# Performance work log

Measured on AMD Instinct MI355X. Metric: run time of the kernel, lower is better.

Reference implementation:

```python
import jax, jax.numpy as jnp
import numpy as np
from jax import lax

B, E, DIN = 16, 1024, 128   # batch, num_edges, link_state_dim
P, D = 2048, 128            # num_paths, path_state_dim


def _topology():
    # deterministic ragged paths: lengths in [4,16], at least one of max length 16
    lengths = 4 + (np.arange(P) % 13)
    idx = np.repeat(np.arange(P), lengths).astype(np.int32)          # path id per entry
    seqs = np.concatenate([np.arange(l) for l in lengths]).astype(np.int32)  # position in path
    paths = np.random.RandomState(0).randint(0, E, size=idx.shape[0]).astype(np.int32)
    return paths, idx, seqs


def setup_inputs() -> dict:
    key = jax.random.key(0)
    ks = jax.random.split(key, 8)
    paths, idx, seqs = _topology()
    s_in = 1.0 / np.sqrt(DIN)
    s_h = 1.0 / np.sqrt(D)
    return dict(
        inputs=jax.random.normal(ks[0], (B, E, DIN), jnp.float32),
        W_in=jax.random.normal(ks[1], (DIN, 3 * D), jnp.float32) * s_in,
        W_rec=jax.random.normal(ks[2], (D, 3 * D), jnp.float32) * s_h,
        b_in=jnp.zeros((3 * D,), jnp.float32),
        b_rec=jnp.zeros((3 * D,), jnp.float32),
        wq=jax.random.normal(ks[3], (D, D), jnp.float32) * s_h,
        wk=jax.random.normal(ks[4], (D, D), jnp.float32) * s_h,
        wv=jax.random.normal(ks[5], (D, D), jnp.float32) * s_h,
        paths=paths, idx=idx, seqs=seqs,
    )


def _forward(inputs, W_in, W_rec, b_in, b_rec, wq, wk, wv, paths, idx, seqs, max_len):
    Bc = inputs.shape[0]
    # --- ragged gather -> dense zero-padded tensor [B, P, max_len, DIN] (tf.gather + scatter_nd) ---
    h_tild = inputs[:, paths]                                  # [B, n_entries, DIN]
    link = jnp.zeros((Bc, P, max_len, DIN), inputs.dtype)
    link = link.at[:, idx, seqs].set(h_tild)
    x = link.reshape(Bc * P, max_len, DIN)                     # [BP, L, DIN]
    # --- GRU over time (keras GRUCell default: reset_after=True, tanh/sigmoid) ---
    xg = jnp.einsum('nld,de->lne', x, W_in) + b_in             # [L, BP, 3D]
    h0 = jnp.zeros((Bc * P, D), inputs.dtype)

    def step(h, xg_t):
        hg = h @ W_rec + b_rec                                 # [BP, 3D]
        xz, xr, xh = jnp.split(xg_t, 3, axis=-1)
        hz, hr, hh = jnp.split(hg, 3, axis=-1)
        z = jax.nn.sigmoid(xz + hz)
        r = jax.nn.sigmoid(xr + hr)
        hc = jnp.tanh(xh + r * hh)
        hn = z * h + (1.0 - z) * hc
        return hn, hn

    last, hs = lax.scan(step, h0, xg)                          # last:[BP,D], hs:[L,BP,D]
    hs = jnp.transpose(hs, (1, 0, 2))                          # [BP, L, D]
    # --- single-query QKV attention (raw scores, no softmax, as in source) ---
    key_ = hs @ wk                                             # [BP, L, D]
    val = hs @ wv                                              # [BP, L, D]
    q = last @ wq                                              # [BP, D]
    att = jnp.einsum('nld,nd->nl', key_, q)                    # [BP, L]
    ctx = jnp.einsum('nl,nld->nd', att, val)                   # [BP, D]
    return ctx.reshape(Bc, P, D)


def reference(inputs, W_in, W_rec, b_in, b_rec, wq, wk, wv, paths, idx, seqs):
    max_len = int(np.max(np.asarray(seqs))) + 1                # static (16)
    return _forward(inputs, W_in, W_rec, b_in, b_rec, wq, wk, wv, paths, idx, seqs, max_len)
```

## Files before the change

### kernel.cpp

```cpp
#include <hip/hip_runtime.h>
#include <hip/hip_bf16.h>
#include <cstddef>

#define P_ 2048
#define B_ 16
#define E_ 1024
#define D_ 128
#define L_ 16
#define TD_ 384

typedef _Float16 f16x2 __attribute__((ext_vector_type(2)));
typedef _Float16 f16x8 __attribute__((ext_vector_type(8)));
typedef float    f32x4 __attribute__((ext_vector_type(4)));

__device__ __forceinline__ unsigned short f2h(float x) {
    _Float16 h = (_Float16)x;
    return __builtin_bit_cast(unsigned short, h);
}
__device__ __forceinline__ unsigned pk2(float a, float b) {
    return __builtin_bit_cast(unsigned, __builtin_amdgcn_cvt_pkrtz(a, b));
}

__device__ __forceinline__ void wf16(const float* __restrict__ src,
                                     unsigned short* __restrict__ dst, int g, int N) {
    int lane = g & 63, kt = (g >> 6) & 3, tile = g >> 8;
    int k0 = kt * 32 + (lane >> 4) * 8;
    int c = tile * 16 + (lane & 15);
#pragma unroll
    for (int j = 0; j < 8; ++j)
        dst[(size_t)g * 8 + j] = f2h(src[(size_t)(k0 + j) * N + c]);
}

__global__ __launch_bounds__(256) void k_prep(const float* __restrict__ W_rec,
                                              const float* __restrict__ W_in,
                                              const float* __restrict__ wq,
                                              const float* __restrict__ wk,
                                              const float* __restrict__ wv,
                                              int* __restrict__ pt,
                                              unsigned short* __restrict__ WfR,
                                              unsigned short* __restrict__ WfI,
                                              unsigned short* __restrict__ wvf,
                                              float* __restrict__ M) {
    __shared__ float wk_lds[128 * 129];
    __shared__ float wq_row2[2][128];
    int blk = blockIdx.x, tid = threadIdx.x;
    if      (blk < 128) { pt[blk * 256 + tid] = -1; return; }
    else if (blk < 152) { wf16(W_rec, WfR, (blk - 128) * 256 + tid, TD_); return; }
    else if (blk < 176) { wf16(W_in,  WfI, (blk - 152) * 256 + tid, TD_); return; }
    else if (blk < 184) { wf16(wv,    wvf, (blk - 176) * 256 + tid, 128); return; }
    int j0 = (blk - 184) * 2;
    int d = tid & 127, half = tid >> 7;
    for (int r = half * 64; r < half * 64 + 64; ++r)
        wk_lds[r * 129 + d] = wk[r * 128 + d];
    wq_row2[half][d] = wq[(j0 + half) * 128 + d];
    __syncthreads();
    float acc = 0.f;
    for (int k = 0; k < 128; ++k) acc += wq_row2[half][k] * wk_lds[d * 129 + k];
    M[(j0 + half) * 128 + d] = acc;
}

__global__ __launch_bounds__(256) void k_G(const float* __restrict__ inputs,
                                           const unsigned short* __restrict__ WfI,
                                           const float* __restrict__ b_in,
                                           unsigned short* __restrict__ G2,
                                           const int* __restrict__ paths,
                                           const int* __restrict__ idx,
                                           const int* __restrict__ seqs, int J, int scatB,
                                           int* __restrict__ pt,
                                           const float* __restrict__ M,
                                           unsigned short* __restrict__ Mf) {
    if (blockIdx.x >= 1024) {
        int tb = blockIdx.x - 1024;
        if (tb < scatB) {
            int j = tb * 256 + threadIdx.x;
            if (j < J) pt[idx[j] * L_ + seqs[j]] = paths[j];
        } else {
            wf16(M, Mf, (tb - scatB) * 256 + threadIdx.x, 128);
        }
        return;
    }
    __shared__ __align__(16) unsigned short a_lds[16][136];
    int tid = threadIdx.x, w = tid >> 6, L = tid & 63;
    int l15 = L & 15, q = L >> 4;
    int row0 = blockIdx.x * 16;
    {
        int r = tid >> 4, c = (tid & 15) * 8;
        const float4* p = (const float4*)(inputs + (size_t)(row0 + r) * 128 + c);
        float4 v0 = p[0], v1 = p[1];
        uint4 st;
        st.x = pk2(v0.x, v0.y); st.y = pk2(v0.z, v0.w);
        st.z = pk2(v1.x, v1.y); st.w = pk2(v1.z, v1.w);
        *(uint4*)&a_lds[r][c] = st;
    }
    __syncthreads();
    f16x8 af[4];
#pragma unroll
    for (int kt = 0; kt < 4; ++kt)
        af[kt] = *(const f16x8*)&a_lds[l15][kt * 32 + q * 8];
#pragma unroll
    for (int ct = 0; ct < 6; ++ct) {
        int tl = 6 * w + ct;
        f32x4 acc = (f32x4){0.f, 0.f, 0.f, 0.f};
#pragma unroll
        for (int kt = 0; kt < 4; ++kt)
            acc = __builtin_amdgcn_mfma_f32_16x16x32_f16(
                af[kt], *(const f16x8*)(WfI + (size_t)((tl * 4 + kt) * 64 + L) * 8), acc, 0, 0, 0);
        int g  = tl >> 3;
        int dd = (tl & 7) * 16 + l15;
        float bia = b_in[tl * 16 + l15];
#pragma unroll
        for (int j = 0; j < 4; ++j) {
            int r = q * 4 + j;
            G2[((size_t)(row0 + r) * 128 + dd) * 4 + g] = f2h(acc[j] + bia);
        }
    }
}

__global__ __launch_bounds__(512, 4) void k_rec(const unsigned short* __restrict__ WfR,
                                                const float* __restrict__ b_rec,
                                                const float* __restrict__ b_in,
                                                const unsigned short* __restrict__ G2,
                                                const int* __restrict__ pt,
                                                const unsigned short* __restrict__ Mf,
                                                const unsigned short* __restrict__ wvf,
                                                float* __restrict__ out) {
    __shared__ __align__(16) unsigned short hsl[16][16][136];
    __shared__ __align__(16) unsigned short qkb[16][136];
    __shared__ __align__(16) unsigned short svb[16][136];
    __shared__ float attl[16][20];
    __shared__ int pt_lds[16][16];

    int tid = threadIdx.x, w = tid >> 6, L = tid & 63;
    int l15 = L & 15, q = L >> 4;
    int c = 16 * w + l15;
    int n0 = blockIdx.x * 16;
    int b  = n0 >> 11;
    int p0 = n0 & (P_ - 1);

    f16x8 bfrag[3][4];
#pragma unroll
    for (int g = 0; g < 3; ++g)
#pragma unroll
        for (int kt = 0; kt < 4; ++kt)
            bfrag[g][kt] = *(const f16x8*)(WfR + (size_t)(((g * 8 + w) * 4 + kt) * 64 + L) * 8);

    if (tid < 256) pt_lds[tid >> 4][tid & 15] = pt[p0 * L_ + tid];

    float bz = b_in[c], br = b_in[128 + c], bh = b_in[256 + c];
    float rz = b_rec[c], rr = b_rec[128 + c], rh = b_rec[256 + c];
    float h_reg[4];
#pragma unroll
    for (int i = 0; i < 4; ++i) h_reg[i] = 0.f;
    __syncthreads();

    const unsigned short* g2b = G2 + (size_t)b * E_ * 512 + (size_t)c * 4;

    uint2 cur[4];
#pragma unroll
    for (int j = 0; j < 4; ++j) {
        int e = pt_lds[q * 4 + j][0];
        cur[j] = make_uint2(0u, 0u);
        if (e >= 0) cur[j] = *(const uint2*)(g2b + (size_t)e * 512);
    }

    for (int t = 0; t < L_; ++t) {
        uint2 nxt[4];
#pragma unroll
        for (int j = 0; j < 4; ++j) nxt[j] = make_uint2(0u, 0u);
        if (t < 15) {
#pragma unroll
            for (int j = 0; j < 4; ++j) {
                int e = pt_lds[q * 4 + j][t + 1];
                if (e >= 0) nxt[j] = *(const uint2*)(g2b + (size_t)e * 512);
            }
        }

        f32x4 acc[3];
#pragma unroll
        for (int g = 0; g < 3; ++g) acc[g] = (f32x4){0.f, 0.f, 0.f, 0.f};
        if (t > 0) {
            f16x8 af[4];
#pragma unroll
            for (int kt = 0; kt < 4; ++kt)
                af[kt] = *(const f16x8*)&hsl[t - 1][l15][kt * 32 + q * 8];
#pragma unroll
            for (int g = 0; g < 3; ++g)
#pragma unroll
                for (int kt = 0; kt < 4; ++kt)
                    acc[g] = __builtin_amdgcn_mfma_f32_16x16x32_f16(af[kt], bfrag[g][kt], acc[g], 0, 0, 0);
        }

#pragma unroll
        for (int j = 0; j < 4; ++j) {
            int row = q * 4 + j;
            int e = pt_lds[row][t];
            float xz, xr, xh;
            if (e >= 0) {
                f16x2 zr = __builtin_bit_cast(f16x2, cur[j].x);
                f16x2 hp = __builtin_bit_cast(f16x2, cur[j].y);
                xz = (float)zr[0]; xr = (float)zr[1]; xh = (float)hp[0];
            } else {
                xz = bz; xr = br; xh = bh;
            }
            float z   = __builtin_amdgcn_rcpf(1.f + __expf(-(xz + acc[0][j] + rz)));
            float rg  = __builtin_amdgcn_rcpf(1.f + __expf(-(xr + acc[1][j] + rr)));
            float pre = xh + rg * (acc[2][j] + rh);
            float hc  = 1.f - 2.f * __builtin_amdgcn_rcpf(__expf(2.f * pre) + 1.f);
            float hn  = hc + z * (h_reg[j] - hc);
            h_reg[j] = hn;
            hsl[t][row][c] = f2h(hn);
            cur[j] = nxt[j];
        }
        __syncthreads();
    }

    {
        f16x8 af[4];
#pragma unroll
        for (int kt = 0; kt < 4; ++kt)
            af[kt] = *(const f16x8*)&hsl[15][l15][kt * 32 + q * 8];
        f32x4 acc = (f32x4){0.f, 0.f, 0.f, 0.f};
#pragma unroll
        for (int kt = 0; kt < 4; ++kt)
            acc = __builtin_amdgcn_mfma_f32_16x16x32_f16(
                af[kt], *(const f16x8*)(Mf + (size_t)((w * 4 + kt) * 64 + L) * 8), acc, 0, 0, 0);
#pragma unroll
        for (int j = 0; j < 4; ++j)
            qkb[q * 4 + j][c] = f2h(acc[j]);
    }
    __syncthreads();

    if (tid < 256) {
        int s = tid & 15, l = tid >> 4;
        const unsigned short* hr = &hsl[l][s][0];
        const unsigned short* qr = &qkb[s][0];
        float a = 0.f;
#pragma unroll
        for (int k = 0; k < 128; k += 2) {
            f16x2 hh = *(const f16x2*)(hr + k);
            f16x2 qq = *(const f16x2*)(qr + k);
            a += (float)hh[0] * (float)qq[0] + (float)hh[1] * (float)qq[1];
        }
        attl[s][l] = a;
    }
    __syncthreads();

    {
        int s = tid >> 5, d0 = (tid & 31) * 4;
        float v[4] = {0.f, 0.f, 0.f, 0.f};
#pragma unroll
        for (int l = 0; l < 16; ++l) {
            float a = attl[s][l];
            f16x2 h0 = *(const f16x2*)&hsl[l][s][d0];
            f16x2 h1 = *(const f16x2*)&hsl[l][s][d0 + 2];
            v[0] += a * (float)h0[0]; v[1] += a * (float)h0[1];
            v[2] += a * (float)h1[0]; v[3] += a * (float)h1[1];
        }
        uint2 st;
        st.x = pk2(v[0], v[1]); st.y = pk2(v[2], v[3]);
        *(uint2*)&svb[s][d0] = st;
    }
    __syncthreads();

    {
        f16x8 af[4];
#pragma unroll
        for (int kt = 0; kt < 4; ++kt)
            af[kt] = *(const f16x8*)&svb[l15][kt * 32 + q * 8];
        f32x4 acc = (f32x4){0.f, 0.f, 0.f, 0.f};
#pragma unroll
        for (int kt = 0; kt < 4; ++kt)
            acc = __builtin_amdgcn_mfma_f32_16x16x32_f16(
                af[kt], *(const f16x8*)(wvf + (size_t)((w * 4 + kt) * 64 + L) * 8), acc, 0, 0, 0);
#pragma unroll
        for (int j = 0; j < 4; ++j)
            out[(size_t)(n0 + q * 4 + j) * D_ + c] = acc[j];
    }
}

extern "C" void kernel_launch(void* const* d_in, const int* in_sizes, int n_in,
                              void* d_out, int out_size, void* d_ws, size_t ws_size,
                              hipStream_t stream) {
    const float* inputs = (const float*)d_in[0];
    const float* W_in   = (const float*)d_in[1];
    const float* W_rec  = (const float*)d_in[2];
    const float* b_in   = (const float*)d_in[3];
    const float* b_rec  = (const float*)d_in[4];
    const float* wq     = (const float*)d_in[5];
    const float* wk     = (const float*)d_in[6];
    const float* wvp    = (const float*)d_in[7];
    const int* paths    = (const int*)d_in[8];
    const int* idx      = (const int*)d_in[9];
    const int* seqs     = (const int*)d_in[10];
    int J = in_sizes[8];

    const size_t off_pt  = 0;
    const size_t off_WfR = off_pt  + (size_t)P_ * L_ * 4;
    const size_t off_WfI = off_WfR + (size_t)24 * 256 * 16;
    const size_t off_Mf  = off_WfI + (size_t)24 * 256 * 16;
    const size_t off_wvf = off_Mf  + (size_t)8 * 256 * 16;
    const size_t off_M   = off_wvf + (size_t)8 * 256 * 16;
    const size_t off_G2  = off_M   + (size_t)128 * 128 * 4;
    char* ws = (char*)d_ws;
    int* pt             = (int*)(ws + off_pt);
    unsigned short* WfR = (unsigned short*)(ws + off_WfR);
    unsigned short* WfI = (unsigned short*)(ws + off_WfI);
    unsigned short* Mf  = (unsigned short*)(ws + off_Mf);
    unsigned short* wvf = (unsigned short*)(ws + off_wvf);
    float* M            = (float*)(ws + off_M);
    unsigned short* G2  = (unsigned short*)(ws + off_G2);
    float* out = (float*)d_out;

    int scatB = (J + 255) / 256;
    k_prep<<<dim3(248), dim3(256), 0, stream>>>(W_rec, W_in, wq, wk, wvp, pt,
                                                WfR, WfI, wvf, M);
    k_G<<<dim3(1024 + scatB + 8), dim3(256), 0, stream>>>(inputs, WfI, b_in, G2,
                                                          paths, idx, seqs, J, scatB,
                                                          pt, M, Mf);
    k_rec<<<dim3(B_ * P_ / 16), dim3(512), 0, stream>>>(WfR, b_rec, b_in, G2, pt,
                                                        Mf, wvf, out);
}
```

Baseline: 208.4 us.

## Add sentinel padding row to G2, transpose recurrent MFMA, fold biases, vectorize loads

```diff
diff --git a/kernel.cpp b/kernel.cpp
--- a/kernel.cpp
+++ b/kernel.cpp
@@ -19,6 +19,22 @@
 }
 __device__ __forceinline__ unsigned pk2(float a, float b) {
     return __builtin_bit_cast(unsigned, __builtin_amdgcn_cvt_pkrtz(a, b));
+}
+__device__ __forceinline__ float lo16(unsigned u) {
+    return (float)__builtin_bit_cast(f16x2, u)[0];
+}
+__device__ __forceinline__ float hi16(unsigned u) {
+    return (float)__builtin_bit_cast(f16x2, u)[1];
+}
+__device__ __forceinline__ float dot2w(unsigned hu, unsigned qu, float c) {
+#if __has_builtin(__builtin_amdgcn_fdot2)
+    typedef __fp16 h2v __attribute__((ext_vector_type(2)));
+    return __builtin_amdgcn_fdot2(__builtin_bit_cast(h2v, hu),
+                                  __builtin_bit_cast(h2v, qu), c, false);
+#else
+    f16x2 h = __builtin_bit_cast(f16x2, hu), q = __builtin_bit_cast(f16x2, qu);
+    return c + (float)h[0] * (float)q[0] + (float)h[1] * (float)q[1];
+#endif
 }
 
 __device__ __forceinline__ void wf16(const float* __restrict__ src,
@@ -44,7 +60,7 @@
     __shared__ float wk_lds[128 * 129];
     __shared__ float wq_row2[2][128];
     int blk = blockIdx.x, tid = threadIdx.x;
-    if      (blk < 128) { pt[blk * 256 + tid] = -1; return; }
+    if      (blk < 128) { pt[blk * 256 + tid] = E_; return; }
     else if (blk < 152) { wf16(W_rec, WfR, (blk - 128) * 256 + tid, TD_); return; }
     else if (blk < 176) { wf16(W_in,  WfI, (blk - 152) * 256 + tid, TD_); return; }
     else if (blk < 184) { wf16(wv,    wvf, (blk - 176) * 256 + tid, 128); return; }
@@ -62,6 +78,7 @@
 __global__ __launch_bounds__(256) void k_G(const float* __restrict__ inputs,
                                            const unsigned short* __restrict__ WfI,
                                            const float* __restrict__ b_in,
+                                           const float* __restrict__ b_rec,
                                            unsigned short* __restrict__ G2,
                                            const int* __restrict__ paths,
                                            const int* __restrict__ idx,
@@ -74,8 +91,17 @@
         if (tb < scatB) {
             int j = tb * 256 + threadIdx.x;
             if (j < J) pt[idx[j] * L_ + seqs[j]] = paths[j];
+        } else if (tb < scatB + 8) {
+            wf16(M, Mf, (tb - scatB) * 256 + threadIdx.x, 128);
         } else {
-            wf16(M, Mf, (tb - scatB) * 256 + threadIdx.x, 128);
+            for (int i = threadIdx.x; i < 2048; i += 256) {
+                int bx = i >> 7, cc = i & 127;
+                size_t base = ((size_t)(bx * (E_ + 1) + E_) * 128 + cc) * 4;
+                G2[base]     = f2h(b_in[cc] + b_rec[cc]);
+                G2[base + 1] = f2h(b_in[128 + cc] + b_rec[128 + cc]);
+                G2[base + 2] = f2h(b_in[256 + cc]);
+                G2[base + 3] = 0;
+            }
         }
         return;
     }
@@ -83,6 +109,7 @@
     int tid = threadIdx.x, w = tid >> 6, L = tid & 63;
     int l15 = L & 15, q = L >> 4;
     int row0 = blockIdx.x * 16;
+    int badd = row0 >> 10;
     {
         int r = tid >> 4, c = (tid & 15) * 8;
         const float4* p = (const float4*)(inputs + (size_t)(row0 + r) * 128 + c);
@@ -107,18 +134,17 @@
                 af[kt], *(const f16x8*)(WfI + (size_t)((tl * 4 + kt) * 64 + L) * 8), acc, 0, 0, 0);
         int g  = tl >> 3;
         int dd = (tl & 7) * 16 + l15;
-        float bia = b_in[tl * 16 + l15];
+        float bia = b_in[tl * 16 + l15] + (g < 2 ? b_rec[tl * 16 + l15] : 0.f);
 #pragma unroll
         for (int j = 0; j < 4; ++j) {
             int r = q * 4 + j;
-            G2[((size_t)(row0 + r) * 128 + dd) * 4 + g] = f2h(acc[j] + bia);
+            G2[((size_t)(row0 + r + badd) * 128 + dd) * 4 + g] = f2h(acc[j] + bia);
         }
     }
 }
 
 __global__ __launch_bounds__(512, 4) void k_rec(const unsigned short* __restrict__ WfR,
                                                 const float* __restrict__ b_rec,
-                                                const float* __restrict__ b_in,
                                                 const unsigned short* __restrict__ G2,
                                                 const int* __restrict__ pt,
                                                 const unsigned short* __restrict__ Mf,
@@ -128,118 +154,113 @@
     __shared__ __align__(16) unsigned short qkb[16][136];
     __shared__ __align__(16) unsigned short svb[16][136];
     __shared__ float attl[16][20];
-    __shared__ int pt_lds[16][16];
+    __shared__ int ofs_lds[16][16];
 
     int tid = threadIdx.x, w = tid >> 6, L = tid & 63;
     int l15 = L & 15, q = L >> 4;
-    int c = 16 * w + l15;
+    int c0 = 16 * w + 4 * q;
     int n0 = blockIdx.x * 16;
     int b  = n0 >> 11;
     int p0 = n0 & (P_ - 1);
-
-    f16x8 bfrag[3][4];
+    int bb = b * (E_ + 1);
+
+    f16x8 afw[3][4];
 #pragma unroll
     for (int g = 0; g < 3; ++g)
 #pragma unroll
         for (int kt = 0; kt < 4; ++kt)
-            bfrag[g][kt] = *(const f16x8*)(WfR + (size_t)(((g * 8 + w) * 4 + kt) * 64 + L) * 8);
-
-    if (tid < 256) pt_lds[tid >> 4][tid & 15] = pt[p0 * L_ + tid];
-
-    float bz = b_in[c], br = b_in[128 + c], bh = b_in[256 + c];
-    float rz = b_rec[c], rr = b_rec[128 + c], rh = b_rec[256 + c];
-    float h_reg[4];
-#pragma unroll
-    for (int i = 0; i < 4; ++i) h_reg[i] = 0.f;
-    __syncthreads();
-
-    const unsigned short* g2b = G2 + (size_t)b * E_ * 512 + (size_t)c * 4;
-
-    uint2 cur[4];
-#pragma unroll
-    for (int j = 0; j < 4; ++j) {
-        int e = pt_lds[q * 4 + j][0];
-        cur[j] = make_uint2(0u, 0u);
-        if (e >= 0) cur[j] = *(const uint2*)(g2b + (size_t)e * 512);
+            afw[g][kt] = *(const f16x8*)(WfR + (size_t)(((g * 8 + w) * 4 + kt) * 64 + L) * 8);
+
+    if (tid < 256)
+        ofs_lds[tid >> 4][tid & 15] = (bb + pt[p0 * L_ + tid]) << 10;
+
+    f32x4 rh4;
+#pragma unroll
+    for (int j = 0; j < 4; ++j) rh4[j] = b_rec[256 + c0 + j];
+    float h_reg[4] = {0.f, 0.f, 0.f, 0.f};
+    __syncthreads();
+
+    const char* g2c = (const char*)G2 + (size_t)c0 * 8;
+    uint4 cur0, cur1;
+    {
+        int off = ofs_lds[l15][0];
+        cur0 = *(const uint4*)(g2c + off);
+        cur1 = *(const uint4*)(g2c + off + 16);
     }
 
     for (int t = 0; t < L_; ++t) {
-        uint2 nxt[4];
-#pragma unroll
-        for (int j = 0; j < 4; ++j) nxt[j] = make_uint2(0u, 0u);
+        uint4 nx0 = cur0, nx1 = cur1;
         if (t < 15) {
-#pragma unroll
-            for (int j = 0; j < 4; ++j) {
-                int e = pt_lds[q * 4 + j][t + 1];
-                if (e >= 0) nxt[j] = *(const uint2*)(g2b + (size_t)e * 512);
-            }
-        }
-
+            int off = ofs_lds[l15][t + 1];
+            nx0 = *(const uint4*)(g2c + off);
+            nx1 = *(const uint4*)(g2c + off + 16);
+        }
+
+        float xh[4];
         f32x4 acc[3];
-#pragma unroll
-        for (int g = 0; g < 3; ++g) acc[g] = (f32x4){0.f, 0.f, 0.f, 0.f};
+        acc[0][0] = lo16(cur0.x); acc[0][1] = lo16(cur0.z);
+        acc[0][2] = lo16(cur1.x); acc[0][3] = lo16(cur1.z);
+        acc[1][0] = hi16(cur0.x); acc[1][1] = hi16(cur0.z);
+        acc[1][2] = hi16(cur1.x); acc[1][3] = hi16(cur1.z);
+        xh[0] = lo16(cur0.y); xh[1] = lo16(cur0.w);
+        xh[2] = lo16(cur1.y); xh[3] = lo16(cur1.w);
+        acc[2] = rh4;
+
         if (t > 0) {
-            f16x8 af[4];
+            f16x8 hf[4];
 #pragma unroll
             for (int kt = 0; kt < 4; ++kt)
-                af[kt] = *(const f16x8*)&hsl[t - 1][l15][kt * 32 + q * 8];
+                hf[kt] = *(const f16x8*)&hsl[t - 1][l15][kt * 32 + q * 8];
 #pragma unroll
             for (int g = 0; g < 3; ++g)
 #pragma unroll
                 for (int kt = 0; kt < 4; ++kt)
-                    acc[g] = __builtin_amdgcn_mfma_f32_16x16x32_f16(af[kt], bfrag[g][kt], acc[g], 0, 0, 0);
-        }
-
+                    acc[g] = __builtin_amdgcn_mfma_f32_16x16x32_f16(afw[g][kt], hf[kt], acc[g], 0, 0, 0);
+        }
+
+        float hn[4];
 #pragma unroll
         for (int j = 0; j < 4; ++j) {
-            int row = q * 4 + j;
-            int e = pt_lds[row][t];
-            float xz, xr, xh;
-            if (e >= 0) {
-                f16x2 zr = __builtin_bit_cast(f16x2, cur[j].x);
-                f16x2 hp = __builtin_bit_cast(f16x2, cur[j].y);
-                xz = (float)zr[0]; xr = (float)zr[1]; xh = (float)hp[0];
-            } else {
-                xz = bz; xr = br; xh = bh;
-            }
-            float z   = __builtin_amdgcn_rcpf(1.f + __expf(-(xz + acc[0][j] + rz)));
-            float rg  = __builtin_amdgcn_rcpf(1.f + __expf(-(xr + acc[1][j] + rr)));
-            float pre = xh + rg * (acc[2][j] + rh);
+            float z   = __builtin_amdgcn_rcpf(1.f + __expf(-acc[0][j]));
+            float rg  = __builtin_amdgcn_rcpf(1.f + __expf(-acc[1][j]));
+            float pre = xh[j] + rg * acc[2][j];
             float hc  = 1.f - 2.f * __builtin_amdgcn_rcpf(__expf(2.f * pre) + 1.f);
-            float hn  = hc + z * (h_reg[j] - hc);
-            h_reg[j] = hn;
-            hsl[t][row][c] = f2h(hn);
-            cur[j] = nxt[j];
-        }
+            hn[j] = hc + z * (h_reg[j] - hc);
+            h_reg[j] = hn[j];
+        }
+        uint2 st;
+        st.x = pk2(hn[0], hn[1]); st.y = pk2(hn[2], hn[3]);
+        *(uint2*)&hsl[t][l15][c0] = st;
+        cur0 = nx0; cur1 = nx1;
         __syncthreads();
     }
 
     {
-        f16x8 af[4];
-#pragma unroll
-        for (int kt = 0; kt < 4; ++kt)
-            af[kt] = *(const f16x8*)&hsl[15][l15][kt * 32 + q * 8];
-        f32x4 acc = (f32x4){0.f, 0.f, 0.f, 0.f};
-#pragma unroll
-        for (int kt = 0; kt < 4; ++kt)
-            acc = __builtin_amdgcn_mfma_f32_16x16x32_f16(
-                af[kt], *(const f16x8*)(Mf + (size_t)((w * 4 + kt) * 64 + L) * 8), acc, 0, 0, 0);
-#pragma unroll
-        for (int j = 0; j < 4; ++j)
-            qkb[q * 4 + j][c] = f2h(acc[j]);
+        f16x8 hf[4];
+#pragma unroll
+        for (int kt = 0; kt < 4; ++kt)
+            hf[kt] = *(const f16x8*)&hsl[15][l15][kt * 32 + q * 8];
+        f32x4 a = (f32x4){0.f, 0.f, 0.f, 0.f};
+#pragma unroll
+        for (int kt = 0; kt < 4; ++kt)
+            a = __builtin_amdgcn_mfma_f32_16x16x32_f16(
+                *(const f16x8*)(Mf + (size_t)((w * 4 + kt) * 64 + L) * 8), hf[kt], a, 0, 0, 0);
+        uint2 st;
+        st.x = pk2(a[0], a[1]); st.y = pk2(a[2], a[3]);
+        *(uint2*)&qkb[l15][c0] = st;
     }
     __syncthreads();
 
     if (tid < 256) {
         int s = tid & 15, l = tid >> 4;
-        const unsigned short* hr = &hsl[l][s][0];
-        const unsigned short* qr = &qkb[s][0];
+        const uint4* hr = (const uint4*)&hsl[l][s][0];
+        const uint4* qr = (const uint4*)&qkb[s][0];
         float a = 0.f;
 #pragma unroll
-        for (int k = 0; k < 128; k += 2) {
-            f16x2 hh = *(const f16x2*)(hr + k);
-            f16x2 qq = *(const f16x2*)(qr + k);
-            a += (float)hh[0] * (float)qq[0] + (float)hh[1] * (float)qq[1];
+        for (int k8 = 0; k8 < 16; ++k8) {
+            uint4 hh = hr[k8], qq = qr[k8];
+            a = dot2w(hh.x, qq.x, a); a = dot2w(hh.y, qq.y, a);
+            a = dot2w(hh.z, qq.z, a); a = dot2w(hh.w, qq.w, a);
         }
         attl[s][l] = a;
     }
@@ -251,10 +272,9 @@
 #pragma unroll
         for (int l = 0; l < 16; ++l) {
             float a = attl[s][l];
-            f16x2 h0 = *(const f16x2*)&hsl[l][s][d0];
-            f16x2 h1 = *(const f16x2*)&hsl[l][s][d0 + 2];
-            v[0] += a * (float)h0[0]; v[1] += a * (float)h0[1];
-            v[2] += a * (float)h1[0]; v[3] += a * (float)h1[1];
+            uint2 hu = *(const uint2*)&hsl[l][s][d0];
+            v[0] += a * lo16(hu.x); v[1] += a * hi16(hu.x);
+            v[2] += a * lo16(hu.y); v[3] += a * hi16(hu.y);
         }
         uint2 st;
         st.x = pk2(v[0], v[1]); st.y = pk2(v[2], v[3]);
@@ -263,18 +283,16 @@
     __syncthreads();
 
     {
-        f16x8 af[4];
-#pragma unroll
-        for (int kt = 0; kt < 4; ++kt)
-            af[kt] = *(const f16x8*)&svb[l15][kt * 32 + q * 8];
-        f32x4 acc = (f32x4){0.f, 0.f, 0.f, 0.f};
-#pragma unroll
-        for (int kt = 0; kt < 4; ++kt)
-            acc = __builtin_amdgcn_mfma_f32_16x16x32_f16(
-                af[kt], *(const f16x8*)(wvf + (size_t)((w * 4 + kt) * 64 + L) * 8), acc, 0, 0, 0);
-#pragma unroll
-        for (int j = 0; j < 4; ++j)
-            out[(size_t)(n0 + q * 4 + j) * D_ + c] = acc[j];
+        f16x8 sf[4];
+#pragma unroll
+        for (int kt = 0; kt < 4; ++kt)
+            sf[kt] = *(const f16x8*)&svb[l15][kt * 32 + q * 8];
+        f32x4 a = (f32x4){0.f, 0.f, 0.f, 0.f};
+#pragma unroll
+        for (int kt = 0; kt < 4; ++kt)
+            a = __builtin_amdgcn_mfma_f32_16x16x32_f16(
+                *(const f16x8*)(wvf + (size_t)((w * 4 + kt) * 64 + L) * 8), sf[kt], a, 0, 0, 0);
+        *(f32x4*)&out[(size_t)(n0 + l15) * D_ + c0] = a;
     }
 }
 
@@ -314,9 +332,9 @@
     int scatB = (J + 255) / 256;
     k_prep<<<dim3(248), dim3(256), 0, stream>>>(W_rec, W_in, wq, wk, wvp, pt,
                                                 WfR, WfI, wvf, M);
-    k_G<<<dim3(1024 + scatB + 8), dim3(256), 0, stream>>>(inputs, WfI, b_in, G2,
-                                                          paths, idx, seqs, J, scatB,
-                                                          pt, M, Mf);
-    k_rec<<<dim3(B_ * P_ / 16), dim3(512), 0, stream>>>(WfR, b_rec, b_in, G2, pt,
+    k_G<<<dim3(1024 + scatB + 8 + 1), dim3(256), 0, stream>>>(inputs, WfI, b_in, b_rec,
+                                                              G2, paths, idx, seqs, J,
+                                                              scatB, pt, M, Mf);
+    k_rec<<<dim3(B_ * P_ / 16), dim3(512), 0, stream>>>(WfR, b_rec, G2, pt,
                                                         Mf, wvf, out);
 }
```

New measurement: 186.1 us. -10.7%, faster.
